# Optimization experiments

Hardware: AMD Instinct MI355X
Metric: run time of the kernel (lower is better)

Reference implementation:

```python
import jax, jax.numpy as jnp
import numpy as np

B, S, D = 1024, 256, 256  # batch, n_class, feature dim (g = n_component = 1)


def setup_inputs() -> dict:
    key = jax.random.key(0)
    k1, k2, k3 = jax.random.split(key, 3)
    x = jax.random.normal(k1, (B, D), dtype=jnp.float32)
    mu_p = jax.random.normal(k2, (S, 1, D), dtype=jnp.float32)
    sigma_p = jax.random.normal(k3, (S, 1, D, D), dtype=jnp.float32)
    return {"x": x, "mu_p": mu_p, "sigma_p": sigma_p}


def _log_probs(x, mu_p, sigma_p):
    sp = sigma_p[:, 0]            # (S, D, D), component index g=0
    mu = mu_p[:, 0]               # (S, D)
    # parameter_enforcing: m = sigma_p^T @ sigma_p (PSD);
    # mean of (real) eigenvalues of m == trace(m)/D, so the ridge term is
    # 0.01 * (trace(m)/D) * I, making sigma symmetric positive definite.
    m = jnp.einsum('skd,ske->sde', sp, sp)                      # (S, D, D)
    ridge = 0.01 * (jnp.trace(m, axis1=-2, axis2=-1) / D)       # (S,)
    sigma = m + ridge[:, None, None] * jnp.eye(D, dtype=m.dtype)
    # MVN log_prob via Cholesky: logdet = 2*sum(log diag L),
    # maha = || L^{-1} (x - mu) ||^2
    L = jnp.linalg.cholesky(sigma)                              # (S, D, D)
    logdet = 2.0 * jnp.sum(jnp.log(jnp.diagonal(L, axis1=-2, axis2=-1)), -1)  # (S,)
    diff = x[None, :, :] - mu[:, None, :]                       # (S, B, D)
    # batched triangular solve per class: y = L^{-1} diff^T -> (S, D, B)
    y = jax.vmap(lambda Ls, ds: jax.scipy.linalg.solve_triangular(Ls, ds.T, lower=True))(L, diff)
    maha = jnp.sum(y * y, axis=1)                               # (S, B)
    log2pi = jnp.log(2.0 * jnp.pi).astype(x.dtype)
    logp = -0.5 * (D * log2pi + logdet[:, None] + maha)         # (S, B)
    return logp.T                                               # (B, S)


def reference(x, mu_p, sigma_p):
    return _log_probs(x, mu_p, sigma_p)
```

## Files before the change

kernel.cpp:

```cpp
#include <hip/hip_runtime.h>
#include <math.h>


#define LOG2PI_D 470.4965290007924f

typedef __attribute__((ext_vector_type(8))) short bf16x8;
typedef __attribute__((ext_vector_type(4))) float f32x4;

__device__ __forceinline__ unsigned bf16rtn(float f) {
  unsigned u = __float_as_uint(f);
  return (u + 0x7FFFu + ((u >> 16) & 1u)) >> 16;
}
__device__ __forceinline__ unsigned packhl(float v) {
  unsigned h = bf16rtn(v);
  float hf = __uint_as_float(h << 16);
  unsigned l = bf16rtn(v - hf);
  return (h << 16) | l;
}
__device__ __forceinline__ void unpack8(unsigned u0, unsigned u1, unsigned u2, unsigned u3,
                                        unsigned u4, unsigned u5, unsigned u6, unsigned u7,
                                        bf16x8* h, bf16x8* l) {
  unsigned uu[8] = {u0, u1, u2, u3, u4, u5, u6, u7};
#pragma unroll
  for (int j = 0; j < 8; ++j) {
    (*h)[j] = (short)(uu[j] >> 16);
    (*l)[j] = (short)(uu[j] & 0xffffu);
  }
}

__global__ __launch_bounds__(256) void k_gram(const float* __restrict__ sp,
                                              float* __restrict__ L,
                                              float* __restrict__ ridge_out) {
  __shared__ unsigned Tr[2 * 128 * 33];
  unsigned* TrA = Tr;
  unsigned* TrB = Tr + 128 * 33;
  int p = blockIdx.y, s = blockIdx.x;
  int bi = (p ? 128 : 0), bj = (p == 2 ? 128 : 0);
  const float* A = sp + (size_t)s * 65536;
  float* C = L + (size_t)s * 65536;
  int tid = threadIdx.x, w = tid >> 6, lane = tid & 63;
  int q = lane >> 4, n = lane & 15;
  int mt0 = 2 * w;
  f32x4 acc[2][8] = {};
  int sr = tid >> 3, sc0 = (tid & 7) * 4;

  float4 va[4], vb[4];
#pragma unroll
  for (int pass = 0; pass < 4; ++pass) {
    int c = sc0 + pass * 32;
    va[pass] = *(const float4*)(A + (size_t)sr * 256 + bi + c);
    if (p == 1) vb[pass] = *(const float4*)(A + (size_t)sr * 256 + bj + c);
  }

  for (int ks = 0; ks < 8; ++ks) {
    __syncthreads();
#pragma unroll
    for (int pass = 0; pass < 4; ++pass) {
      int c = sc0 + pass * 32;
      TrA[(c + 0) * 33 + sr] = packhl(va[pass].x);
      TrA[(c + 1) * 33 + sr] = packhl(va[pass].y);
      TrA[(c + 2) * 33 + sr] = packhl(va[pass].z);
      TrA[(c + 3) * 33 + sr] = packhl(va[pass].w);
      if (p == 1) {
        TrB[(c + 0) * 33 + sr] = packhl(vb[pass].x);
        TrB[(c + 1) * 33 + sr] = packhl(vb[pass].y);
        TrB[(c + 2) * 33 + sr] = packhl(vb[pass].z);
        TrB[(c + 3) * 33 + sr] = packhl(vb[pass].w);
      }
    }
    __syncthreads();
    if (ks < 7) {
#pragma unroll
      for (int pass = 0; pass < 4; ++pass) {
        int c = sc0 + pass * 32;
        va[pass] = *(const float4*)(A + (size_t)((ks + 1) * 32 + sr) * 256 + bi + c);
        if (p == 1)
          vb[pass] = *(const float4*)(A + (size_t)((ks + 1) * 32 + sr) * 256 + bj + c);
      }
    }
    const unsigned* TB = (p == 1) ? TrB : TrA;
    bf16x8 Ah[2], Al[2];
#pragma unroll
    for (int t = 0; t < 2; ++t) {
      const unsigned* ap = &TrA[((mt0 + t) * 16 + n) * 33 + q * 8];
      uint4 a0 = *(const uint4*)ap;
      uint4 a1 = *(const uint4*)(ap + 4);
      unpack8(a0.x, a0.y, a0.z, a0.w, a1.x, a1.y, a1.z, a1.w, &Ah[t], &Al[t]);
    }
    int ntmax = (p == 1) ? 8 : (mt0 + 2);
    for (int nt = 0; nt < ntmax; ++nt) {
      const unsigned* bp = &TB[(nt * 16 + n) * 33 + q * 8];
      uint4 b0v = *(const uint4*)bp;
      uint4 b1v = *(const uint4*)(bp + 4);
      bf16x8 bh, bl;
      unpack8(b0v.x, b0v.y, b0v.z, b0v.w, b1v.x, b1v.y, b1v.z, b1v.w, &bh, &bl);
#pragma unroll
      for (int t = 0; t < 2; ++t) {
        if (p == 1 || nt <= mt0 + t) {
          acc[t][nt] = __builtin_amdgcn_mfma_f32_16x16x32_bf16(Ah[t], bh, acc[t][nt], 0, 0, 0);
          acc[t][nt] = __builtin_amdgcn_mfma_f32_16x16x32_bf16(Ah[t], bl, acc[t][nt], 0, 0, 0);
          acc[t][nt] = __builtin_amdgcn_mfma_f32_16x16x32_bf16(Al[t], bh, acc[t][nt], 0, 0, 0);
        }
      }
    }
  }
  if (p != 1) {
    float dsum = 0.f;
#pragma unroll
    for (int t = 0; t < 2; ++t) {
      int mt = mt0 + t;
      if ((n >> 2) == q) dsum += acc[t][mt][n & 3];
    }
    dsum += __shfl_down(dsum, 32, 64);
    dsum += __shfl_down(dsum, 16, 64);
    dsum += __shfl_down(dsum, 8, 64);
    dsum += __shfl_down(dsum, 4, 64);
    dsum += __shfl_down(dsum, 2, 64);
    dsum += __shfl_down(dsum, 1, 64);
    if (lane == 0) atomicAdd(&ridge_out[s], dsum * (0.01f / 256.0f));
  }
  float* slab = (float*)Tr;
  for (int t = 0; t < 2; ++t) {
    __syncthreads();
#pragma unroll
    for (int nt = 0; nt < 8; ++nt)
#pragma unroll
      for (int r = 0; r < 4; ++r)
        slab[w * 2048 + (q * 4 + r) * 128 + nt * 16 + n] = acc[t][nt][r];
    __syncthreads();
#pragma unroll
    for (int it = 0; it < 8; ++it) {
      int idx = tid + it * 256;
      int row = idx >> 5, c4 = idx & 31;
      int wsrc = row >> 4, r16 = row & 15;
      int d = bi + (2 * wsrc + t) * 16 + r16;
      *(float4*)(C + (size_t)d * 256 + bj + c4 * 4) =
          *(float4*)&slab[wsrc * 2048 + r16 * 128 + c4 * 4];
    }
  }
}

__global__ __launch_bounds__(256) void k_panel(float* __restrict__ L,
                                               const float* __restrict__ ridge_buf,
                                               int kb) {
  extern __shared__ float lds[];
  float* P = lds;
  float* W = lds + 64 * 68;
  float* WT = lds + 2 * 64 * 68;
  float* T = lds + 3 * 64 * 68;
  int s = blockIdx.x;
  float* M = L + (size_t)s * 65536;
  int tid = threadIdx.x;
  int k4 = tid & 15, rb = tid >> 4;
  int ty = tid >> 4, tx = tid & 15;
  int base = kb * 64;
  float ridge = ridge_buf[s];

  for (int r = rb; r < 64; r += 16)
    *(float4*)&P[r * 68 + k4 * 4] = *(const float4*)(M + (size_t)(base + r) * 256 + base + k4 * 4);
  __syncthreads();
  if (tid < 64) P[tid * 68 + tid] += ridge;
  __syncthreads();
  {
    int eo = tid & 63, ro = tid >> 6;
    for (int cb = 0; cb < 16; ++cb) {
      int c0 = cb * 4;
      float g00 = P[c0 * 68 + c0];
      float g10 = P[(c0 + 1) * 68 + c0], g11 = P[(c0 + 1) * 68 + c0 + 1];
      float g20 = P[(c0 + 2) * 68 + c0], g21 = P[(c0 + 2) * 68 + c0 + 1],
            g22 = P[(c0 + 2) * 68 + c0 + 2];
      float g30 = P[(c0 + 3) * 68 + c0], g31 = P[(c0 + 3) * 68 + c0 + 1],
            g32 = P[(c0 + 3) * 68 + c0 + 2], g33 = P[(c0 + 3) * 68 + c0 + 3];
      float l00 = sqrtf(g00), r0 = 1.f / l00;
      float l10 = g10 * r0, l20 = g20 * r0, l30 = g30 * r0;
      float l11 = sqrtf(g11 - l10 * l10), r1 = 1.f / l11;
      float l21 = (g21 - l20 * l10) * r1, l31 = (g31 - l30 * l10) * r1;
      float l22 = sqrtf(g22 - l20 * l20 - l21 * l21), r2 = 1.f / l22;
      float l32 = (g32 - l30 * l20 - l31 * l21) * r2;
      float l33 = sqrtf(g33 - l30 * l30 - l31 * l31 - l32 * l32), r3 = 1.f / l33;
      int e = c0 + 4 + eo;
      if (e < 64) {
        float p0 = P[e * 68 + c0], p1 = P[e * 68 + c0 + 1];
        float p2 = P[e * 68 + c0 + 2], p3 = P[e * 68 + c0 + 3];
        float le0 = p0 * r0;
        float le1 = (p1 - le0 * l10) * r1;
        float le2 = (p2 - le0 * l20 - le1 * l21) * r2;
        float le3 = (p3 - le0 * l30 - le1 * l31 - le2 * l32) * r3;
        for (int r = c0 + 4 + ro; r < 64; r += 4) {
          float q0 = P[r * 68 + c0], q1 = P[r * 68 + c0 + 1];
          float q2 = P[r * 68 + c0 + 2], q3 = P[r * 68 + c0 + 3];
          float lr0 = q0 * r0;
          float lr1 = (q1 - lr0 * l10) * r1;
          float lr2 = (q2 - lr0 * l20 - lr1 * l21) * r2;
          float lr3 = (q3 - lr0 * l30 - lr1 * l31 - lr2 * l32) * r3;
          P[r * 68 + e] -= lr0 * le0 + lr1 * le1 + lr2 * le2 + lr3 * le3;
        }
      }
      __syncthreads();
    }
  }
  {
    int cb = tid >> 4, lane16 = tid & 15;
    int c0 = cb * 4;
    float g00 = P[c0 * 68 + c0];
    float g10 = P[(c0 + 1) * 68 + c0], g11 = P[(c0 + 1) * 68 + c0 + 1];
    float g20 = P[(c0 + 2) * 68 + c0], g21 = P[(c0 + 2) * 68 + c0 + 1],
          g22 = P[(c0 + 2) * 68 + c0 + 2];
    float g30 = P[(c0 + 3) * 68 + c0], g31 = P[(c0 + 3) * 68 + c0 + 1],
          g32 = P[(c0 + 3) * 68 + c0 + 2], g33 = P[(c0 + 3) * 68 + c0 + 3];
    float l00 = sqrtf(g00), r0 = 1.f / l00;
    float l10 = g10 * r0, l20 = g20 * r0, l30 = g30 * r0;
    float l11 = sqrtf(g11 - l10 * l10), r1 = 1.f / l11;
    float l21 = (g21 - l20 * l10) * r1, l31 = (g31 - l30 * l10) * r1;
    float l22 = sqrtf(g22 - l20 * l20 - l21 * l21), r2 = 1.f / l22;
    float l32 = (g32 - l30 * l20 - l31 * l21) * r2;
    float l33 = sqrtf(g33 - l30 * l30 - l31 * l31 - l32 * l32), r3 = 1.f / l33;
    float vals[4][4];
    int rows[4], nr = 0;
    for (int r = c0 + lane16; r < 64; r += 16) {
      int i = r - c0;
      if (i == 0) { vals[nr][0] = l00; vals[nr][1] = 0; vals[nr][2] = 0; vals[nr][3] = 0; }
      else if (i == 1) { vals[nr][0] = l10; vals[nr][1] = l11; vals[nr][2] = 0; vals[nr][3] = 0; }
      else if (i == 2) { vals[nr][0] = l20; vals[nr][1] = l21; vals[nr][2] = l22; vals[nr][3] = 0; }
      else if (i == 3) { vals[nr][0] = l30; vals[nr][1] = l31; vals[nr][2] = l32; vals[nr][3] = l33; }
      else {
        float q0 = P[r * 68 + c0], q1 = P[r * 68 + c0 + 1];
        float q2 = P[r * 68 + c0 + 2], q3 = P[r * 68 + c0 + 3];
        float lr0 = q0 * r0;
        float lr1 = (q1 - lr0 * l10) * r1;
        float lr2 = (q2 - lr0 * l20 - lr1 * l21) * r2;
        float lr3 = (q3 - lr0 * l30 - lr1 * l31 - lr2 * l32) * r3;
        vals[nr][0] = lr0; vals[nr][1] = lr1; vals[nr][2] = lr2; vals[nr][3] = lr3;
      }
      rows[nr++] = r;
    }
    __syncthreads();
    for (int u = 0; u < nr; ++u) {
      int r = rows[u];
      P[r * 68 + c0] = vals[u][0];
      P[r * 68 + c0 + 1] = vals[u][1];
      P[r * 68 + c0 + 2] = vals[u][2];
      P[r * 68 + c0 + 3] = vals[u][3];
    }
  }
  __syncthreads();
  if (tid < 64) {
    int c = tid;
    int rl = (c < 32) ? 32 : 64;
    for (int r = 0; r < c; ++r) W[r * 68 + c] = 0.f;
    W[c * 68 + c] = 1.0f / P[c * 68 + c];
    for (int r = c + 1; r < rl; ++r) {
      float a = 0.f;
      for (int k = c; k < r; ++k) a += P[r * 68 + k] * W[k * 68 + c];
      W[r * 68 + c] = -a / P[r * 68 + r];
    }
  }
  __syncthreads();
  {
    int r0 = (tid >> 4) * 2, c0 = (tid & 15) * 2;
    float a00 = 0, a01 = 0, a10 = 0, a11 = 0;
    for (int k = 0; k < 32; ++k) {
      float b0 = P[(32 + r0) * 68 + k], b1 = P[(33 + r0) * 68 + k];
      float w0 = W[k * 68 + c0], w1 = W[k * 68 + c0 + 1];
      a00 += b0 * w0; a01 += b0 * w1; a10 += b1 * w0; a11 += b1 * w1;
    }
    T[r0 * 68 + c0] = a00; T[r0 * 68 + c0 + 1] = a01;
    T[(r0 + 1) * 68 + c0] = a10; T[(r0 + 1) * 68 + c0 + 1] = a11;
  }
  __syncthreads();
  {
    int r0 = (tid >> 4) * 2, c0 = (tid & 15) * 2;
    float a00 = 0, a01 = 0, a10 = 0, a11 = 0;
    for (int k = 0; k < 32; ++k) {
      float i0 = W[(32 + r0) * 68 + 32 + k], i1 = W[(33 + r0) * 68 + 32 + k];
      float t0 = T[k * 68 + c0], t1 = T[k * 68 + c0 + 1];
      a00 += i0 * t0; a01 += i0 * t1; a10 += i1 * t0; a11 += i1 * t1;
    }
    W[(32 + r0) * 68 + c0] = -a00; W[(32 + r0) * 68 + c0 + 1] = -a01;
    W[(33 + r0) * 68 + c0] = -a10; W[(33 + r0) * 68 + c0 + 1] = -a11;
  }
  __syncthreads();
  for (int c = rb; c < 64; c += 16) {
    float4 v = *(float4*)&W[c * 68 + k4 * 4];
    WT[(k4 * 4 + 0) * 68 + c] = v.x;
    WT[(k4 * 4 + 1) * 68 + c] = v.y;
    WT[(k4 * 4 + 2) * 68 + c] = v.z;
    WT[(k4 * 4 + 3) * 68 + c] = v.w;
  }
  __syncthreads();
  for (int r = rb; r < 64; r += 16)
    *(float4*)(M + (size_t)(base + r) * 256 + base + k4 * 4) = *(float4*)&W[r * 68 + k4 * 4];
  int nrt = 3 - kb;
  for (int rt = 0; rt < nrt; ++rt) {
    int g0 = base + 64 + rt * 64;
    __syncthreads();
    for (int r = rb; r < 64; r += 16) {
      float4 v = *(const float4*)(M + (size_t)(g0 + r) * 256 + base + k4 * 4);
      T[(k4 * 4 + 0) * 68 + r] = v.x;
      T[(k4 * 4 + 1) * 68 + r] = v.y;
      T[(k4 * 4 + 2) * 68 + r] = v.z;
      T[(k4 * 4 + 3) * 68 + r] = v.w;
    }
    __syncthreads();
    float acc[4][4] = {};
    for (int k = 0; k < 64; ++k) {
      float a[4], b[4];
      *(float4*)a = *(float4*)&T[k * 68 + ty * 4];
      *(float4*)b = *(float4*)&WT[k * 68 + tx * 4];
#pragma unroll
      for (int i = 0; i < 4; ++i)
#pragma unroll
        for (int j = 0; j < 4; ++j) acc[i][j] += a[i] * b[j];
    }
    __syncthreads();
#pragma unroll
    for (int i = 0; i < 4; ++i)
      *(float4*)(M + (size_t)(g0 + ty * 4 + i) * 256 + base + tx * 4) =
          make_float4(acc[i][0], acc[i][1], acc[i][2], acc[i][3]);
#pragma unroll
    for (int i = 0; i < 4; ++i)
#pragma unroll
      for (int j = 0; j < 4; ++j) T[(tx * 4 + j) * 68 + ty * 4 + i] = acc[i][j];
    __syncthreads();
    for (int r = rb; r < 64; r += 16)
      *(float4*)(M + (size_t)(base + r) * 256 + g0 + k4 * 4) = *(float4*)&T[r * 68 + k4 * 4];
  }
}

__global__ __launch_bounds__(256) void k_trail(float* __restrict__ L, int kb) {
  extern __shared__ float lds[];
  float* Pi = lds;
  float* Pj = lds + 64 * 68;
  int p = blockIdx.y, s = blockIdx.x;
  int ti = 0, tj = 0, cnt = 0;
  for (int a = kb + 1; a < 4; ++a)
    for (int b = kb + 1; b <= a; ++b) {
      if (cnt == p) { ti = a; tj = b; }
      ++cnt;
    }
  float* M = L + (size_t)s * 65536;
  int tid = threadIdx.x, k4 = tid & 15, rb = tid >> 4;
  int ty = tid >> 4, tx = tid & 15;
  int base = kb * 64;
  for (int k = rb; k < 64; k += 16) {
    *(float4*)&Pi[k * 68 + k4 * 4] = *(const float4*)(M + (size_t)(base + k) * 256 + ti * 64 + k4 * 4);
    *(float4*)&Pj[k * 68 + k4 * 4] = *(const float4*)(M + (size_t)(base + k) * 256 + tj * 64 + k4 * 4);
  }
  float acc[4][4];
#pragma unroll
  for (int i = 0; i < 4; ++i)
    *(float4*)&acc[i][0] = *(const float4*)(M + (size_t)(ti * 64 + ty * 4 + i) * 256 + tj * 64 + tx * 4);
  __syncthreads();
  for (int k = 0; k < 64; ++k) {
    float a[4], b[4];
    *(float4*)a = *(float4*)&Pi[k * 68 + ty * 4];
    *(float4*)b = *(float4*)&Pj[k * 68 + tx * 4];
#pragma unroll
    for (int i = 0; i < 4; ++i)
#pragma unroll
      for (int j = 0; j < 4; ++j) acc[i][j] -= a[i] * b[j];
  }
#pragma unroll
  for (int i = 0; i < 4; ++i)
    *(float4*)(M + (size_t)(ti * 64 + ty * 4 + i) * 256 + tj * 64 + tx * 4) =
        make_float4(acc[i][0], acc[i][1], acc[i][2], acc[i][3]);
}

__global__ __launch_bounds__(256) void k_invcol(float* __restrict__ Lw) {
  extern __shared__ float lds[];
  float* Bcol = lds;
  float* LW = lds + 3 * 64 * 68;
  float* Cs = LW + 64 * 68;
  int j = blockIdx.y, s = blockIdx.x;
  float* M = Lw + (size_t)s * 65536;
  unsigned* M32 = (unsigned*)M;
  int tid = threadIdx.x, k4 = tid & 15, rb = tid >> 4;
  int ty = tid >> 4, tx = tid & 15;

  for (int r = rb; r < 64; r += 16)
    *(float4*)&Bcol[r * 68 + k4 * 4] =
        *(const float4*)(M + (size_t)(j * 64 + r) * 256 + j * 64 + k4 * 4);
  __syncthreads();

  for (int i = j + 1; i < 4; ++i) {
    float acc[4][4] = {};
    for (int kk = j; kk < i; ++kk) {
      __syncthreads();
      for (int k = rb; k < 64; k += 16)
        *(float4*)&LW[k * 68 + k4 * 4] =
            *(const float4*)(M + (size_t)(kk * 64 + k) * 256 + i * 64 + k4 * 4);
      __syncthreads();
      float* Bk = Bcol + (kk - j) * 64 * 68;
#pragma unroll 4
      for (int k = 0; k < 64; ++k) {
        float a[4], b[4];
        *(float4*)a = *(float4*)&LW[k * 68 + ty * 4];
        *(float4*)b = *(float4*)&Bk[k * 68 + tx * 4];
#pragma unroll
        for (int r = 0; r < 4; ++r)
#pragma unroll
          for (int c = 0; c < 4; ++c) acc[r][c] += a[r] * b[c];
      }
    }
    __syncthreads();
#pragma unroll
    for (int r = 0; r < 4; ++r)
      *(float4*)&Cs[(ty * 4 + r) * 68 + tx * 4] =
          make_float4(acc[r][0], acc[r][1], acc[r][2], acc[r][3]);
    for (int r = rb; r < 64; r += 16) {
      float4 v = *(const float4*)(M + (size_t)(i * 64 + r) * 256 + i * 64 + k4 * 4);
      LW[(k4 * 4 + 0) * 68 + r] = v.x;
      LW[(k4 * 4 + 1) * 68 + r] = v.y;
      LW[(k4 * 4 + 2) * 68 + r] = v.z;
      LW[(k4 * 4 + 3) * 68 + r] = v.w;
    }
    __syncthreads();
    float d[4][4] = {};
#pragma unroll 4
    for (int k = 0; k < 64; ++k) {
      float a[4], b[4];
      *(float4*)a = *(float4*)&LW[k * 68 + ty * 4];
      *(float4*)b = *(float4*)&Cs[k * 68 + tx * 4];
#pragma unroll
      for (int r = 0; r < 4; ++r)
#pragma unroll
        for (int c = 0; c < 4; ++c) d[r][c] -= a[r] * b[c];
    }
    float* Bi = Bcol + (i - j) * 64 * 68;
#pragma unroll
    for (int r = 0; r < 4; ++r) {
      if (i < 3)
        *(float4*)&Bi[(ty * 4 + r) * 68 + tx * 4] =
            make_float4(d[r][0], d[r][1], d[r][2], d[r][3]);
      uint4 pu;
      pu.x = packhl(d[r][0]); pu.y = packhl(d[r][1]);
      pu.z = packhl(d[r][2]); pu.w = packhl(d[r][3]);
      *(uint4*)(M32 + (size_t)(i * 64 + ty * 4 + r) * 256 + j * 64 + tx * 4) = pu;
    }
    __syncthreads();
  }
}

__global__ __launch_bounds__(512) void k_maha(const float* __restrict__ x,
                                              const float* __restrict__ mu_p,
                                              const float* __restrict__ Lw,
                                              float* __restrict__ out) {
  __shared__ __align__(16) short Bh[128 * 40];
  __shared__ __align__(16) short Bl[128 * 40];
  __shared__ float Red[1025];
  int s = blockIdx.x, b0 = blockIdx.y * 128;
  const float* Mf = Lw + (size_t)s * 65536;
  const unsigned* M32 = (const unsigned*)Mf;
  int tid = threadIdx.x, w = tid >> 6, lane = tid & 63;
  int q = lane >> 4, n = lane & 15;
  int mt_[2] = {w, 15 - w};
  f32x4 acc[2][8] = {};

  for (int ks = 0; ks < 8; ++ks) {
    __syncthreads();
    {
      int b = tid >> 2, q8 = tid & 3;
      const float* xp = x + (size_t)(b0 + b) * 256 + ks * 32 + q8 * 8;
      const float* mp = mu_p + (size_t)s * 256 + ks * 32 + q8 * 8;
      float4 xa = ((const float4*)xp)[0], xb = ((const float4*)xp)[1];
      float4 ma = ((const float4*)mp)[0], mb = ((const float4*)mp)[1];
      float dv[8] = {xa.x - ma.x, xa.y - ma.y, xa.z - ma.z, xa.w - ma.w,
                     xb.x - mb.x, xb.y - mb.y, xb.z - mb.z, xb.w - mb.w};
      unsigned h[8], l[8];
#pragma unroll
      for (int jj = 0; jj < 8; ++jj) {
        h[jj] = bf16rtn(dv[jj]);
        float hf = __uint_as_float(h[jj] << 16);
        l[jj] = bf16rtn(dv[jj] - hf);
      }
      *(uint4*)&Bh[b * 40 + q8 * 8] =
          make_uint4(h[0] | (h[1] << 16), h[2] | (h[3] << 16),
                     h[4] | (h[5] << 16), h[6] | (h[7] << 16));
      *(uint4*)&Bl[b * 40 + q8 * 8] =
          make_uint4(l[0] | (l[1] << 16), l[2] | (l[3] << 16),
                     l[4] | (l[5] << 16), l[6] | (l[7] << 16));
    }
    __syncthreads();
    bf16x8 Ah[2], Al[2];
    bool act[2];
#pragma unroll
    for (int t = 0; t < 2; ++t) {
      int mt = mt_[t];
      act[t] = ks < ((mt + 2) >> 1);
      if (act[t]) {
        const unsigned* ap = M32 + (size_t)(mt * 16 + n) * 256 + ks * 32 + q * 8;
        uint4 u0 = *(const uint4*)ap;
        uint4 u1 = *(const uint4*)(ap + 4);
        unsigned uu[8] = {u0.x, u0.y, u0.z, u0.w, u1.x, u1.y, u1.z, u1.w};
        if ((ks >> 1) == (mt >> 2)) {
#pragma unroll
          for (int jj = 0; jj < 8; ++jj) {
            float f = __uint_as_float(uu[jj]);
            unsigned hh = bf16rtn(f);
            float hf = __uint_as_float(hh << 16);
            Ah[t][jj] = (short)hh;
            Al[t][jj] = (short)bf16rtn(f - hf);
          }
        } else {
#pragma unroll
          for (int jj = 0; jj < 8; ++jj) {
            Ah[t][jj] = (short)(uu[jj] >> 16);
            Al[t][jj] = (short)(uu[jj] & 0xffffu);
          }
        }
      }
    }
#pragma unroll
    for (int bsub = 0; bsub < 8; ++bsub) {
      bf16x8 bh = *(const bf16x8*)&Bh[(bsub * 16 + n) * 40 + q * 8];
      bf16x8 bl = *(const bf16x8*)&Bl[(bsub * 16 + n) * 40 + q * 8];
#pragma unroll
      for (int t = 0; t < 2; ++t) {
        if (act[t]) {
          acc[t][bsub] = __builtin_amdgcn_mfma_f32_16x16x32_bf16(Ah[t], bh, acc[t][bsub], 0, 0, 0);
          acc[t][bsub] = __builtin_amdgcn_mfma_f32_16x16x32_bf16(Ah[t], bl, acc[t][bsub], 0, 0, 0);
          acc[t][bsub] = __builtin_amdgcn_mfma_f32_16x16x32_bf16(Al[t], bh, acc[t][bsub], 0, 0, 0);
        }
      }
    }
  }
#pragma unroll
  for (int bsub = 0; bsub < 8; ++bsub) {
    float v = 0.f;
#pragma unroll
    for (int t = 0; t < 2; ++t)
#pragma unroll
      for (int r = 0; r < 4; ++r) v += acc[t][bsub][r] * acc[t][bsub][r];
    v += __shfl_xor(v, 16, 64);
    v += __shfl_xor(v, 32, 64);
    if (lane < 16) Red[w * 128 + bsub * 16 + lane] = v;
  }
  if (w == 0) {
    float ld = 0.f;
#pragma unroll
    for (int c = 0; c < 4; ++c)
      ld += logf(Mf[(size_t)(c * 64 + lane) * 256 + c * 64 + lane]);
    ld += __shfl_down(ld, 32, 64);
    ld += __shfl_down(ld, 16, 64);
    ld += __shfl_down(ld, 8, 64);
    ld += __shfl_down(ld, 4, 64);
    ld += __shfl_down(ld, 2, 64);
    ld += __shfl_down(ld, 1, 64);
    if (lane == 0) Red[1024] = ld;
  }
  __syncthreads();
  if (tid < 128) {
    float mh = 0.f;
#pragma unroll
    for (int w2 = 0; w2 < 8; ++w2) mh += Red[w2 * 128 + tid];
    out[(size_t)(b0 + tid) * 256 + s] = -0.5f * (LOG2PI_D - 2.0f * Red[1024] + mh);
  }
}

extern "C" void kernel_launch(void* const* d_in, const int* in_sizes, int n_in,
                              void* d_out, int out_size, void* d_ws, size_t ws_size,
                              hipStream_t stream) {
  const float* x = (const float*)d_in[0];
  const float* mu = (const float*)d_in[1];
  const float* sp = (const float*)d_in[2];
  float* out = (float*)d_out;
  float* L = (float*)d_ws;

  const int panel_lds = 4 * 64 * 68 * 4;
  const int trail_lds = 2 * 64 * 68 * 4;
  const int invc_lds = 5 * 64 * 68 * 4;
  (void)hipFuncSetAttribute((const void*)k_panel,
                            hipFuncAttributeMaxDynamicSharedMemorySize, panel_lds);
  (void)hipFuncSetAttribute((const void*)k_trail,
                            hipFuncAttributeMaxDynamicSharedMemorySize, trail_lds);
  (void)hipFuncSetAttribute((const void*)k_invcol,
                            hipFuncAttributeMaxDynamicSharedMemorySize, invc_lds);

  k_gram<<<dim3(256, 3), 256, 0, stream>>>(sp, L, out);
  const int npairs[4] = {6, 3, 1, 0};
  for (int kb = 0; kb < 4; ++kb) {
    k_panel<<<256, 256, panel_lds, stream>>>(L, out, kb);
    if (npairs[kb])
      k_trail<<<dim3(256, npairs[kb]), 256, trail_lds, stream>>>(L, kb);
  }
  k_invcol<<<dim3(256, 3), 256, invc_lds, stream>>>(L);
  k_maha<<<dim3(256, 8), 512, 0, stream>>>(x, mu, L, out);
}
```

Before: 645.8 us.

## Pre-split bf16 hi/lo into separate LDS arrays and balance triangular tiles across waves

The gram kernel now splits each fp32 value into packed bf16 hi and lo parts when staging, and stores them in separate LDS arrays laid out so MFMA operands load directly as bf16x8 vectors, with no per-iteration unpacking. Global loads change to per-column scalar loads over 16 rows. Row tiles are assigned as w and 7-w so the triangular diagonal blocks give each wave equal work. Stores above the diagonal are skipped. The scalar global loads may coalesce differently, and the strided LDS writes could cause bank conflicts.

```diff
diff --git a/kernel.cpp b/kernel.cpp
--- a/kernel.cpp
+++ b/kernel.cpp
@@ -17,86 +17,90 @@
   unsigned l = bf16rtn(v - hf);
   return (h << 16) | l;
 }
-__device__ __forceinline__ void unpack8(unsigned u0, unsigned u1, unsigned u2, unsigned u3,
-                                        unsigned u4, unsigned u5, unsigned u6, unsigned u7,
-                                        bf16x8* h, bf16x8* l) {
-  unsigned uu[8] = {u0, u1, u2, u3, u4, u5, u6, u7};
-#pragma unroll
-  for (int j = 0; j < 8; ++j) {
-    (*h)[j] = (short)(uu[j] >> 16);
-    (*l)[j] = (short)(uu[j] & 0xffffu);
-  }
-}
 
 __global__ __launch_bounds__(256) void k_gram(const float* __restrict__ sp,
                                               float* __restrict__ L,
                                               float* __restrict__ ridge_out) {
-  __shared__ unsigned Tr[2 * 128 * 33];
-  unsigned* TrA = Tr;
-  unsigned* TrB = Tr + 128 * 33;
+  __shared__ unsigned Hb[4 * 128 * 20];
+  unsigned* AH = Hb;
+  unsigned* AL = Hb + 128 * 20;
+  unsigned* BH = Hb + 2 * 128 * 20;
+  unsigned* BL = Hb + 3 * 128 * 20;
   int p = blockIdx.y, s = blockIdx.x;
   int bi = (p ? 128 : 0), bj = (p == 2 ? 128 : 0);
   const float* A = sp + (size_t)s * 65536;
   float* C = L + (size_t)s * 65536;
   int tid = threadIdx.x, w = tid >> 6, lane = tid & 63;
   int q = lane >> 4, n = lane & 15;
-  int mt0 = 2 * w;
+  int mt_[2] = {w, 7 - w};
   f32x4 acc[2][8] = {};
-  int sr = tid >> 3, sc0 = (tid & 7) * 4;
-
-  float4 va[4], vb[4];
-#pragma unroll
-  for (int pass = 0; pass < 4; ++pass) {
-    int c = sc0 + pass * 32;
-    va[pass] = *(const float4*)(A + (size_t)sr * 256 + bi + c);
-    if (p == 1) vb[pass] = *(const float4*)(A + (size_t)sr * 256 + bj + c);
+  int c = tid & 127, g = tid >> 7;
+
+  float va[16], vb[16];
+#pragma unroll
+  for (int u = 0; u < 16; ++u) {
+    va[u] = A[(size_t)(g * 16 + u) * 256 + bi + c];
+    if (p == 1) vb[u] = A[(size_t)(g * 16 + u) * 256 + bj + c];
   }
 
   for (int ks = 0; ks < 8; ++ks) {
     __syncthreads();
-#pragma unroll
-    for (int pass = 0; pass < 4; ++pass) {
-      int c = sc0 + pass * 32;
-      TrA[(c + 0) * 33 + sr] = packhl(va[pass].x);
-      TrA[(c + 1) * 33 + sr] = packhl(va[pass].y);
-      TrA[(c + 2) * 33 + sr] = packhl(va[pass].z);
-      TrA[(c + 3) * 33 + sr] = packhl(va[pass].w);
+    {
+      unsigned hw[8], lw[8];
+#pragma unroll
+      for (int m = 0; m < 8; ++m) {
+        float v0 = va[2 * m], v1 = va[2 * m + 1];
+        unsigned h0 = bf16rtn(v0), h1 = bf16rtn(v1);
+        float r0 = v0 - __uint_as_float(h0 << 16);
+        float r1 = v1 - __uint_as_float(h1 << 16);
+        hw[m] = h0 | (h1 << 16);
+        lw[m] = bf16rtn(r0) | (bf16rtn(r1) << 16);
+      }
+      *(uint4*)&AH[c * 20 + g * 8] = make_uint4(hw[0], hw[1], hw[2], hw[3]);
+      *(uint4*)&AH[c * 20 + g * 8 + 4] = make_uint4(hw[4], hw[5], hw[6], hw[7]);
+      *(uint4*)&AL[c * 20 + g * 8] = make_uint4(lw[0], lw[1], lw[2], lw[3]);
+      *(uint4*)&AL[c * 20 + g * 8 + 4] = make_uint4(lw[4], lw[5], lw[6], lw[7]);
       if (p == 1) {
-        TrB[(c + 0) * 33 + sr] = packhl(vb[pass].x);
-        TrB[(c + 1) * 33 + sr] = packhl(vb[pass].y);
-        TrB[(c + 2) * 33 + sr] = packhl(vb[pass].z);
-        TrB[(c + 3) * 33 + sr] = packhl(vb[pass].w);
+#pragma unroll
+        for (int m = 0; m < 8; ++m) {
+          float v0 = vb[2 * m], v1 = vb[2 * m + 1];
+          unsigned h0 = bf16rtn(v0), h1 = bf16rtn(v1);
+          float r0 = v0 - __uint_as_float(h0 << 16);
+          float r1 = v1 - __uint_as_float(h1 << 16);
+          hw[m] = h0 | (h1 << 16);
+          lw[m] = bf16rtn(r0) | (bf16rtn(r1) << 16);
+        }
+        *(uint4*)&BH[c * 20 + g * 8] = make_uint4(hw[0], hw[1], hw[2], hw[3]);
+        *(uint4*)&BH[c * 20 + g * 8 + 4] = make_uint4(hw[4], hw[5], hw[6], hw[7]);
+        *(uint4*)&BL[c * 20 + g * 8] = make_uint4(lw[0], lw[1], lw[2], lw[3]);
+        *(uint4*)&BL[c * 20 + g * 8 + 4] = make_uint4(lw[4], lw[5], lw[6], lw[7]);
       }
     }
     __syncthreads();
     if (ks < 7) {
-#pragma unroll
-      for (int pass = 0; pass < 4; ++pass) {
-        int c = sc0 + pass * 32;
-        va[pass] = *(const float4*)(A + (size_t)((ks + 1) * 32 + sr) * 256 + bi + c);
-        if (p == 1)
-          vb[pass] = *(const float4*)(A + (size_t)((ks + 1) * 32 + sr) * 256 + bj + c);
-      }
-    }
-    const unsigned* TB = (p == 1) ? TrB : TrA;
+      int r0g = (ks + 1) * 32 + g * 16;
+#pragma unroll
+      for (int u = 0; u < 16; ++u) {
+        va[u] = A[(size_t)(r0g + u) * 256 + bi + c];
+        if (p == 1) vb[u] = A[(size_t)(r0g + u) * 256 + bj + c];
+      }
+    }
+    const unsigned* TBH = (p == 1) ? BH : AH;
+    const unsigned* TBL = (p == 1) ? BL : AL;
     bf16x8 Ah[2], Al[2];
 #pragma unroll
     for (int t = 0; t < 2; ++t) {
-      const unsigned* ap = &TrA[((mt0 + t) * 16 + n) * 33 + q * 8];
-      uint4 a0 = *(const uint4*)ap;
-      uint4 a1 = *(const uint4*)(ap + 4);
-      unpack8(a0.x, a0.y, a0.z, a0.w, a1.x, a1.y, a1.z, a1.w, &Ah[t], &Al[t]);
-    }
-    int ntmax = (p == 1) ? 8 : (mt0 + 2);
+      int col = mt_[t] * 16 + n;
+      Ah[t] = *(const bf16x8*)&AH[col * 20 + q * 4];
+      Al[t] = *(const bf16x8*)&AL[col * 20 + q * 4];
+    }
+    int ntmax = (p == 1) ? 8 : (8 - w);
     for (int nt = 0; nt < ntmax; ++nt) {
-      const unsigned* bp = &TB[(nt * 16 + n) * 33 + q * 8];
-      uint4 b0v = *(const uint4*)bp;
-      uint4 b1v = *(const uint4*)(bp + 4);
-      bf16x8 bh, bl;
-      unpack8(b0v.x, b0v.y, b0v.z, b0v.w, b1v.x, b1v.y, b1v.z, b1v.w, &bh, &bl);
+      bf16x8 bh = *(const bf16x8*)&TBH[(nt * 16 + n) * 20 + q * 4];
+      bf16x8 bl = *(const bf16x8*)&TBL[(nt * 16 + n) * 20 + q * 4];
 #pragma unroll
       for (int t = 0; t < 2; ++t) {
-        if (p == 1 || nt <= mt0 + t) {
+        if (p == 1 || nt <= mt_[t]) {
           acc[t][nt] = __builtin_amdgcn_mfma_f32_16x16x32_bf16(Ah[t], bh, acc[t][nt], 0, 0, 0);
           acc[t][nt] = __builtin_amdgcn_mfma_f32_16x16x32_bf16(Ah[t], bl, acc[t][nt], 0, 0, 0);
           acc[t][nt] = __builtin_amdgcn_mfma_f32_16x16x32_bf16(Al[t], bh, acc[t][nt], 0, 0, 0);
@@ -108,8 +112,7 @@
     float dsum = 0.f;
 #pragma unroll
     for (int t = 0; t < 2; ++t) {
-      int mt = mt0 + t;
-      if ((n >> 2) == q) dsum += acc[t][mt][n & 3];
+      if ((n >> 2) == q) dsum += acc[t][mt_[t]][n & 3];
     }
     dsum += __shfl_down(dsum, 32, 64);
     dsum += __shfl_down(dsum, 16, 64);
@@ -119,7 +122,7 @@
     dsum += __shfl_down(dsum, 1, 64);
     if (lane == 0) atomicAdd(&ridge_out[s], dsum * (0.01f / 256.0f));
   }
-  float* slab = (float*)Tr;
+  float* slab = (float*)Hb;
   for (int t = 0; t < 2; ++t) {
     __syncthreads();
 #pragma unroll
@@ -133,9 +136,12 @@
       int idx = tid + it * 256;
       int row = idx >> 5, c4 = idx & 31;
       int wsrc = row >> 4, r16 = row & 15;
-      int d = bi + (2 * wsrc + t) * 16 + r16;
-      *(float4*)(C + (size_t)d * 256 + bj + c4 * 4) =
-          *(float4*)&slab[wsrc * 2048 + r16 * 128 + c4 * 4];
+      int rt = t ? (7 - wsrc) : wsrc;
+      if (p == 1 || (c4 >> 2) <= rt) {
+        int d = bi + rt * 16 + r16;
+        *(float4*)(C + (size_t)d * 256 + bj + c4 * 4) =
+            *(float4*)&slab[wsrc * 2048 + r16 * 128 + c4 * 4];
+      }
     }
   }
 }
```

Result: faster. 623.5 us (-3.4%).
